# Kernel tuning notes

Hardware: AMD Instinct MI355X
Metric: run time of the kernel (lower is better)

## Reference

```python
import jax, jax.numpy as jnp
import numpy as np
from jax import lax

VOCAB, E, H = 32000, 256, 512
B, T = 64, 1024


def setup_inputs() -> dict:
    key = jax.random.key(0)
    ks = jax.random.split(key, 5)
    tokens = jax.random.randint(ks[0], (B, T), 0, VOCAB, dtype=jnp.int64 if jax.config.jax_enable_x64 else jnp.int32).astype(jnp.int32)
    emb_table = jax.random.normal(ks[1], (VOCAB, E), dtype=jnp.float32) * 0.02
    W_x = jax.random.normal(ks[2], (E, 4 * H), dtype=jnp.float32) * 0.02
    W_h = jax.random.normal(ks[3], (H, 4 * H), dtype=jnp.float32) * 0.02
    b = jnp.zeros((4 * H,), dtype=jnp.float32)
    h0 = jnp.zeros((B, H), dtype=jnp.float32)
    c0 = jnp.zeros((B, H), dtype=jnp.float32)
    return {"tokens": tokens, "h0": h0, "c0": c0, "emb_table": emb_table,
            "W_x": W_x, "W_h": W_h, "b": b}


def reference(tokens, h0, c0, emb_table, W_x, W_h, b):
    # Embedding lookup with mask_zero=True semantics: token 0 is padding.
    x = emb_table[tokens]                      # [B, T, E]
    mask = tokens != 0                         # [B, T]
    # Precompute input projections for all timesteps (same math, one GEMM).
    xz = jnp.einsum('bte,ef->btf', x, W_x) + b  # [B, T, 4H]

    def step(carry, inp):
        h, c = carry
        xzt, mt = inp                          # [B,4H], [B]
        z = xzt + h @ W_h                      # [B, 4H]
        i, f, g, o = jnp.split(z, 4, axis=-1)  # Keras gate order: i, f, c, o
        i = jax.nn.sigmoid(i)
        f = jax.nn.sigmoid(f)
        g = jnp.tanh(g)
        o = jax.nn.sigmoid(o)
        c_new = f * c + i * g
        h_new = o * jnp.tanh(c_new)
        m = mt[:, None]
        # Masked steps carry previous state/output (Keras masking behavior).
        h = jnp.where(m, h_new, h)
        c = jnp.where(m, c_new, c)
        return (h, c), h

    (h_T, c_T), outs = lax.scan(step, (h0, c0),
                                (xz.transpose(1, 0, 2), mask.T))
    return outs.transpose(1, 0, 2), h_T, c_T  # [B,T,H], [B,H], [B,H]
```

## Files before the change

### kernel.cpp

```cpp
#include <hip/hip_runtime.h>
#include <hip/hip_bf16.h>

#define B_ 64
#define T_ 1024
#define E_ 256
#define H_ 512
#define ZN_ 2048
#define NSLICE 64
#define KTX 8
#define KTH 16
#define KT_ (KTX + KTH)

typedef short bf16x8 __attribute__((ext_vector_type(8)));
typedef float f32x4 __attribute__((ext_vector_type(4)));
typedef int i32x4 __attribute__((ext_vector_type(4)));

union frag_u { i32x4 i; bf16x8 h; };

#define RAW_BAR() __builtin_amdgcn_s_barrier()
#define LGKM0() asm volatile("s_waitcnt lgkmcnt(0)" ::: "memory")
#define VM0() asm volatile("s_waitcnt vmcnt(0)" ::: "memory")
#define SCHED_BAR() __builtin_amdgcn_sched_barrier(0)

__device__ __forceinline__ short f2bf(float f) {
  union { float f; unsigned u; } v; v.f = f;
  unsigned r = v.u + 0x7fffu + ((v.u >> 16) & 1u);
  return (short)(r >> 16);
}
__device__ __forceinline__ float sigmoidf_(float x) { return 1.f / (1.f + __expf(-x)); }
__device__ __forceinline__ float tanhf_(float x) {
  x = fminf(10.f, fmaxf(-10.f, x));
  float e = __expf(2.f * x);
  return (e - 1.f) / (e + 1.f);
}

__device__ __forceinline__ i32x4 ld_sys(const void* p) {
  i32x4 r;
  asm volatile("global_load_dwordx4 %0, %1, off sc0 sc1" : "=v"(r) : "v"(p) : "memory");
  return r;
}
__device__ __forceinline__ i32x4 ld_sys16_poll(const void* p) {
  i32x4 r;
  asm volatile("global_load_dwordx4 %0, %1, off sc0 sc1\n\ts_waitcnt vmcnt(0)"
               : "=v"(r) : "v"(p) : "memory");
  return r;
}
__device__ __forceinline__ void st_sys(void* p, i32x4 v) {
  asm volatile("global_store_dwordx4 %0, %1, off sc0 sc1" :: "v"(p), "v"(v) : "memory");
}
__device__ __forceinline__ void st_sys_i32(int* p, int v) {
  asm volatile("global_store_dword %0, %1, off sc0 sc1" :: "v"(p), "v"(v) : "memory");
}


__global__ void k_emb_cvt(const float* __restrict__ emb, short* __restrict__ dst, int n8) {
  int i = blockIdx.x * blockDim.x + threadIdx.x;
  if (i >= n8) return;
  const float4* s = (const float4*)emb;
  float4 a = s[2 * i], b = s[2 * i + 1];
  bf16x8 o;
  o[0] = f2bf(a.x); o[1] = f2bf(a.y); o[2] = f2bf(a.z); o[3] = f2bf(a.w);
  o[4] = f2bf(b.x); o[5] = f2bf(b.y); o[6] = f2bf(b.z); o[7] = f2bf(b.w);
  ((bf16x8*)dst)[i] = o;
}

__global__ void k_wfrag(const float* __restrict__ Wx, const float* __restrict__ Wh,
                        short* __restrict__ wf) {
  int tid = blockIdx.x * blockDim.x + threadIdx.x;
  if (tid >= NSLICE * 2 * KT_ * 64) return;
  int lane = tid & 63;
  int kt = (tid >> 6) % KT_;
  int nt = (tid >> 6) / KT_ % 2;
  int s = tid / (64 * KT_ * 2);
  int c16 = lane & 15, ksub = lane >> 4;
  int g = c16 & 3, hc = c16 >> 2;
  int zcol = g * H_ + s * 8 + nt * 4 + hc;
  int k0 = kt * 32 + ksub * 8;
  bf16x8 o;
#pragma unroll
  for (int i = 0; i < 8; ++i) {
    int k = k0 + i;
    float v = (k < E_) ? Wx[(size_t)k * ZN_ + zcol] : Wh[(size_t)(k - E_) * ZN_ + zcol];
    o[i] = f2bf(v);
  }
  ((bf16x8*)wf)[tid] = o;
}

__global__ void k_tok(const int* __restrict__ tok, int* __restrict__ tokT,
                      unsigned long long* __restrict__ mask) {
  int t = blockIdx.x * blockDim.x + threadIdx.x;
  if (t >= T_) return;
  unsigned long long m = 0ull;
  for (int b = 0; b < B_; ++b) {
    int tk = tok[b * T_ + t];
    tokT[t * B_ + b] = tk;
    if (tk != 0) m |= (1ull << b);
  }
  mask[t] = m;
}

__global__ void k_init(const float* __restrict__ h0, short* __restrict__ hbuf0,
                       int* __restrict__ flags) {
  int i = blockIdx.x * blockDim.x + threadIdx.x;
  if (i < 1024) flags[i] = 0;
  if (i >= B_ * H_) return;
  hbuf0[i] = f2bf(h0[i]);
}


__global__ __launch_bounds__(384, 1) void k_lstm(
    const int* __restrict__ tokT, const short* __restrict__ emb,
    const short* __restrict__ wf, const float* __restrict__ bias,
    const unsigned long long* __restrict__ maskv,
    short* __restrict__ hb0, short* __restrict__ hb1,
    const float* __restrict__ h0, const float* __restrict__ c0,
    float* __restrict__ out, int* __restrict__ tags)
{
  __shared__ __align__(16) short x_wf[2 * KTX * 64 * 8];
  __shared__ __align__(16) float hlocF[2][B_][8];
  __shared__ __align__(16) short hlocBF[B_][8];
  __shared__ int scnt, ocnt;

  int s = blockIdx.x;
  int w = threadIdx.x >> 6, l = threadIdx.x & 63;
  int c16 = l & 15, ksub = l >> 4;
  int g = c16 & 3, hc = c16 >> 2;
  int base = l & ~3;
  int arow = w * 16 + c16;

  if (threadIdx.x == 0) { scnt = 0; ocnt = 0; }

  for (int idx = threadIdx.x; idx < 2 * KTX * 64; idx += 384) {
    int lane = idx & 63;
    int ktn = idx >> 6;
    int nt = ktn / KTX, kt = ktn % KTX;
    ((bf16x8*)x_wf)[idx] = ((const bf16x8*)wf)[(((size_t)(s * 2 + nt)) * KT_ + kt) * 64 + lane];
  }

  bf16x8 wreg0[KTH], wreg1[KTH];
  float zb0 = 0.f, zb1 = 0.f;
  float cst[2][4], hst[2][4];
  if (w < 4) {
    const bf16x8* b0 = (const bf16x8*)wf + (((size_t)(s * 2 + 0)) * KT_ + KTX) * 64 + l;
    const bf16x8* b1 = (const bf16x8*)wf + (((size_t)(s * 2 + 1)) * KT_ + KTX) * 64 + l;
#pragma unroll
    for (int kt = 0; kt < KTH; ++kt) { wreg0[kt] = b0[kt * 64]; wreg1[kt] = b1[kt * 64]; }
    zb0 = bias[g * H_ + s * 8 + 0 + hc];
    zb1 = bias[g * H_ + s * 8 + 4 + hc];
#pragma unroll
    for (int j = 0; j < 2; ++j) {
      int col = s * 8 + j * 4 + hc;
#pragma unroll
      for (int r = 0; r < 4; ++r) {
        int row = w * 16 + ksub * 4 + r;
        cst[j][r] = c0[row * H_ + col];
        hst[j][r] = h0[row * H_ + col];
      }
    }
  }
  LGKM0();
  RAW_BAR();

  f32x4 accx0 = {0.f, 0.f, 0.f, 0.f}, accx1 = {0.f, 0.f, 0.f, 0.f};
  auto compute_x = [&](int t) {
    int tk = tokT[t * B_ + arow];
    const bf16x8* ax = (const bf16x8*)emb + (size_t)tk * 32 + ksub;
    f32x4 a0 = {0.f, 0.f, 0.f, 0.f}, a1 = {0.f, 0.f, 0.f, 0.f};
#pragma unroll
    for (int kt = 0; kt < KTX; ++kt) {
      bf16x8 a = ax[kt * 4];
      a0 = __builtin_amdgcn_mfma_f32_16x16x32_bf16(a, ((const bf16x8*)x_wf)[(0 * KTX + kt) * 64 + l], a0, 0, 0, 0);
      a1 = __builtin_amdgcn_mfma_f32_16x16x32_bf16(a, ((const bf16x8*)x_wf)[(1 * KTX + kt) * 64 + l], a1, 0, 0, 0);
    }
    accx0 = a0; accx1 = a1;
  };

  if (w < 4) compute_x(0);

  if (w < 4) {
    for (int t = 0; t < T_; ++t) {
      int par = t & 1;
      const short* hr = (t & 1) ? hb1 : hb0;
      short* hw       = (t & 1) ? hb0 : hb1;

      if (t > 0) {
        for (;;) {
          i32x4 tg = ld_sys16_poll(tags + l * 4);
          if (__all(tg[0] >= t && tg[1] >= t && tg[2] >= t && tg[3] >= t)) break;
        }
      }

      const short* hbase = hr + arow * H_ + ksub * 8;
      frag_u hf[KTH];
#pragma unroll
      for (int kt = 0; kt < KTH; ++kt) hf[kt].i = ld_sys(hbase + kt * 32);
      VM0();
      SCHED_BAR();

      f32x4 ac0 = accx0, ac1 = accx1;
#pragma unroll
      for (int kt = 0; kt < KTH; ++kt) {
        ac0 = __builtin_amdgcn_mfma_f32_16x16x32_bf16(hf[kt].h, wreg0[kt], ac0, 0, 0, 0);
        ac1 = __builtin_amdgcn_mfma_f32_16x16x32_bf16(hf[kt].h, wreg1[kt], ac1, 0, 0, 0);
      }

      while (__hip_atomic_load(&ocnt, __ATOMIC_ACQUIRE, __HIP_MEMORY_SCOPE_WORKGROUP) < 2 * (t - 1)) {}

      unsigned long long mk = maskv[t];
#pragma unroll
      for (int j = 0; j < 2; ++j) {
        float zb = (j == 0) ? zb0 : zb1;
        int lc = j * 4 + hc;
        float act[4];
#pragma unroll
        for (int r = 0; r < 4; ++r) {
          float z = ((j == 0) ? ac0[r] : ac1[r]) + zb;
          act[r] = (g == 2) ? tanhf_(z) : sigmoidf_(z);
        }
#pragma unroll
        for (int r = 0; r < 4; ++r) {
          float fs = __shfl(act[r], base + 1);
          float gt = __shfl(act[r], base + 2);
          float os = __shfl(act[r], base + 3);
          if (g == 0) {
            int row = w * 16 + ksub * 4 + r;
            bool mm = (mk >> row) & 1ull;
            float cn = fs * cst[j][r] + act[r] * gt;
            float hn = os * tanhf_(cn);
            if (mm) { cst[j][r] = cn; hst[j][r] = hn; }
            hlocF[par][row][lc] = hst[j][r];
            hlocBF[row][lc] = f2bf(hst[j][r]);
          }
        }
      }
      LGKM0();
      SCHED_BAR();

      if (l == 0)
        __hip_atomic_fetch_add(&scnt, 1, __ATOMIC_RELEASE, __HIP_MEMORY_SCOPE_WORKGROUP);

      if (l < 16) {
        frag_u pv; pv.h = *(const bf16x8*)&hlocBF[w * 16 + l][0];
        st_sys(hw + (w * 16 + l) * H_ + s * 8, pv.i);
      }
      if (t == T_ - 1 && g == 0) {
#pragma unroll
        for (int j = 0; j < 2; ++j) {
          int col = s * 8 + j * 4 + hc;
#pragma unroll
          for (int r = 0; r < 4; ++r) {
            int row = w * 16 + ksub * 4 + r;
            out[(size_t)B_ * T_ * H_ + row * H_ + col] = hst[j][r];
            out[(size_t)B_ * T_ * H_ + B_ * H_ + row * H_ + col] = cst[j][r];
          }
        }
      }
      VM0();
      if (l == 0) st_sys_i32(tags + (s * 4 + w), t + 1);

      if (t + 1 < T_) compute_x(t + 1);
    }
  } else {
    for (int t = 0; t < T_; ++t) {
      int par = t & 1;
      while (__hip_atomic_load(&scnt, __ATOMIC_ACQUIRE, __HIP_MEMORY_SCOPE_WORKGROUP) < 4 * (t + 1)) {}
      int row = (w - 4) * 32 + (l >> 1), half = l & 1;
      f32x4 v = *(const f32x4*)&hlocF[par][row][half * 4];
      LGKM0();
      if (l == 0)
        __hip_atomic_fetch_add(&ocnt, 1, __ATOMIC_RELEASE, __HIP_MEMORY_SCOPE_WORKGROUP);
      __builtin_nontemporal_store(v, (f32x4*)(out + ((size_t)row * T_ + t) * H_ + s * 8 + half * 4));
    }
  }
}


extern "C" void kernel_launch(void* const* d_in, const int* in_sizes, int n_in,
                              void* d_out, int out_size, void* d_ws, size_t ws_size,
                              hipStream_t stream) {
  (void)in_sizes; (void)n_in; (void)out_size; (void)ws_size;
  const int* tokens = (const int*)d_in[0];
  const float* h0 = (const float*)d_in[1];
  const float* c0 = (const float*)d_in[2];
  const float* emb = (const float*)d_in[3];
  const float* Wx = (const float*)d_in[4];
  const float* Wh = (const float*)d_in[5];
  const float* bias = (const float*)d_in[6];
  float* out = (float*)d_out;
  char* ws = (char*)d_ws;

  short* emb_bf = (short*)(ws);
  short* wf     = (short*)(ws + 16384000);
  unsigned long long* mask = (unsigned long long*)(ws + 19529728);
  int* tokT     = (int*)(ws + 19537920);
  short* hb0    = (short*)(ws + 19800064);
  short* hb1    = (short*)(ws + 19865600);
  int* tags     = (int*)(ws + 19931136);

  k_emb_cvt<<<(1024000 + 255) / 256, 256, 0, stream>>>(emb, emb_bf, 1024000);
  k_wfrag<<<(NSLICE * 2 * KT_ * 64 + 255) / 256, 256, 0, stream>>>(Wx, Wh, wf);
  k_tok<<<(T_ + 255) / 256, 256, 0, stream>>>(tokens, tokT, mask);
  k_init<<<(B_ * H_ + 255) / 256, 256, 0, stream>>>(h0, hb0, tags);

  k_lstm<<<NSLICE, 384, 0, stream>>>(tokT, emb_bf, wf, bias, mask,
                                     hb0, hb1, h0, c0, out, tags);
}
```

Baseline: 6.563 ms.

## Embed step epoch tags inside hidden-state packets to remove separate flag polling

Replaces the separate per-wave tag flags and the store-wait-flag sequence with hidden-state packets that carry the step number next to the data. Consumers poll the data itself until every packet shows the current epoch, so the flag write, its memory fence, and one round-trip between blocks drop out of each recurrent step. The recurrent weights move from registers into LDS, which frees registers but adds LDS reads on the critical path. Tokens are stored as 16-bit values. The packets double the bytes stored and loaded per step, and polling re-reads the full h fragment on every retry.

```diff
diff --git a/kernel.cpp b/kernel.cpp
--- a/kernel.cpp
+++ b/kernel.cpp
@@ -39,17 +39,8 @@
   asm volatile("global_load_dwordx4 %0, %1, off sc0 sc1" : "=v"(r) : "v"(p) : "memory");
   return r;
 }
-__device__ __forceinline__ i32x4 ld_sys16_poll(const void* p) {
-  i32x4 r;
-  asm volatile("global_load_dwordx4 %0, %1, off sc0 sc1\n\ts_waitcnt vmcnt(0)"
-               : "=v"(r) : "v"(p) : "memory");
-  return r;
-}
 __device__ __forceinline__ void st_sys(void* p, i32x4 v) {
   asm volatile("global_store_dwordx4 %0, %1, off sc0 sc1" :: "v"(p), "v"(v) : "memory");
-}
-__device__ __forceinline__ void st_sys_i32(int* p, int v) {
-  asm volatile("global_store_dword %0, %1, off sc0 sc1" :: "v"(p), "v"(v) : "memory");
 }
 
 
@@ -86,37 +77,45 @@
   ((bf16x8*)wf)[tid] = o;
 }
 
-__global__ void k_tok(const int* __restrict__ tok, int* __restrict__ tokT,
+__global__ void k_tok(const int* __restrict__ tok, unsigned short* __restrict__ tokT,
                       unsigned long long* __restrict__ mask) {
   int t = blockIdx.x * blockDim.x + threadIdx.x;
   if (t >= T_) return;
   unsigned long long m = 0ull;
   for (int b = 0; b < B_; ++b) {
     int tk = tok[b * T_ + t];
-    tokT[t * B_ + b] = tk;
+    tokT[t * B_ + b] = (unsigned short)tk;
     if (tk != 0) m |= (1ull << b);
   }
   mask[t] = m;
 }
 
-__global__ void k_init(const float* __restrict__ h0, short* __restrict__ hbuf0,
-                       int* __restrict__ flags) {
+__global__ void k_init(const float* __restrict__ h0, int* __restrict__ hx) {
   int i = blockIdx.x * blockDim.x + threadIdx.x;
-  if (i < 1024) flags[i] = 0;
-  if (i >= B_ * H_) return;
-  hbuf0[i] = f2bf(h0[i]);
-}
-
-
-__global__ __launch_bounds__(384, 1) void k_lstm(
-    const int* __restrict__ tokT, const short* __restrict__ emb,
+  if (i >= 2 * B_ * 128) return;
+  int par = i >> 13;
+  int row = (i >> 7) & 63;
+  int cg = i & 127;
+  i32x4 g = {0, 0, 0, 0};
+  if (par == 0) {
+    const float* src = h0 + row * H_ + cg * 4;
+    g[0] = ((int)f2bf(src[0]) & 0xffff) | ((int)f2bf(src[1]) << 16);
+    g[1] = ((int)f2bf(src[2]) & 0xffff) | ((int)f2bf(src[3]) << 16);
+  }
+  ((i32x4*)hx)[i] = g;
+}
+
+
+__global__ __launch_bounds__(384, 2) void k_lstm(
+    const unsigned short* __restrict__ tokT, const short* __restrict__ emb,
     const short* __restrict__ wf, const float* __restrict__ bias,
     const unsigned long long* __restrict__ maskv,
-    short* __restrict__ hb0, short* __restrict__ hb1,
+    int* __restrict__ hx,
     const float* __restrict__ h0, const float* __restrict__ c0,
-    float* __restrict__ out, int* __restrict__ tags)
+    float* __restrict__ out)
 {
   __shared__ __align__(16) short x_wf[2 * KTX * 64 * 8];
+  __shared__ __align__(16) short wh_lds[2 * KTH * 64 * 8];
   __shared__ __align__(16) float hlocF[2][B_][8];
   __shared__ __align__(16) short hlocBF[B_][8];
   __shared__ int scnt, ocnt;
@@ -136,15 +135,16 @@
     int nt = ktn / KTX, kt = ktn % KTX;
     ((bf16x8*)x_wf)[idx] = ((const bf16x8*)wf)[(((size_t)(s * 2 + nt)) * KT_ + kt) * 64 + lane];
   }
-
-  bf16x8 wreg0[KTH], wreg1[KTH];
+  for (int idx = threadIdx.x; idx < 2 * KTH * 64; idx += 384) {
+    int lane = idx & 63;
+    int ktn = idx >> 6;
+    int nt = ktn / KTH, kt = ktn % KTH;
+    ((bf16x8*)wh_lds)[idx] = ((const bf16x8*)wf)[(((size_t)(s * 2 + nt)) * KT_ + KTX + kt) * 64 + lane];
+  }
+
   float zb0 = 0.f, zb1 = 0.f;
   float cst[2][4], hst[2][4];
   if (w < 4) {
-    const bf16x8* b0 = (const bf16x8*)wf + (((size_t)(s * 2 + 0)) * KT_ + KTX) * 64 + l;
-    const bf16x8* b1 = (const bf16x8*)wf + (((size_t)(s * 2 + 1)) * KT_ + KTX) * 64 + l;
-#pragma unroll
-    for (int kt = 0; kt < KTH; ++kt) { wreg0[kt] = b0[kt * 64]; wreg1[kt] = b1[kt * 64]; }
     zb0 = bias[g * H_ + s * 8 + 0 + hc];
     zb1 = bias[g * H_ + s * 8 + 4 + hc];
 #pragma unroll
@@ -178,30 +178,40 @@
   if (w < 4) compute_x(0);
 
   if (w < 4) {
+    const bf16x8* whp = (const bf16x8*)wh_lds;
     for (int t = 0; t < T_; ++t) {
       int par = t & 1;
-      const short* hr = (t & 1) ? hb1 : hb0;
-      short* hw       = (t & 1) ? hb0 : hb1;
-
-      if (t > 0) {
-        for (;;) {
-          i32x4 tg = ld_sys16_poll(tags + l * 4);
-          if (__all(tg[0] >= t && tg[1] >= t && tg[2] >= t && tg[3] >= t)) break;
-        }
-      }
-
-      const short* hbase = hr + arow * H_ + ksub * 8;
+
+      const i32x4* gbase = (const i32x4*)hx + ((size_t)par * B_ + arow) * 128 + ksub * 2;
       frag_u hf[KTH];
-#pragma unroll
-      for (int kt = 0; kt < KTH; ++kt) hf[kt].i = ld_sys(hbase + kt * 32);
-      VM0();
-      SCHED_BAR();
+      for (;;) {
+        i32x4 ga[KTH], gb[KTH];
+#pragma unroll
+        for (int kt = 0; kt < KTH; ++kt) {
+          ga[kt] = ld_sys(gbase + kt * 8);
+          gb[kt] = ld_sys(gbase + kt * 8 + 1);
+        }
+        VM0();
+        SCHED_BAR();
+        bool ok = true;
+#pragma unroll
+        for (int kt = 0; kt < KTH; ++kt)
+          ok = ok && ga[kt][2] >= t && gb[kt][2] >= t;
+        if (__all(ok)) {
+#pragma unroll
+          for (int kt = 0; kt < KTH; ++kt) {
+            i32x4 f = {ga[kt][0], ga[kt][1], gb[kt][0], gb[kt][1]};
+            hf[kt].i = f;
+          }
+          break;
+        }
+      }
 
       f32x4 ac0 = accx0, ac1 = accx1;
 #pragma unroll
       for (int kt = 0; kt < KTH; ++kt) {
-        ac0 = __builtin_amdgcn_mfma_f32_16x16x32_bf16(hf[kt].h, wreg0[kt], ac0, 0, 0, 0);
-        ac1 = __builtin_amdgcn_mfma_f32_16x16x32_bf16(hf[kt].h, wreg1[kt], ac1, 0, 0, 0);
+        ac0 = __builtin_amdgcn_mfma_f32_16x16x32_bf16(hf[kt].h, whp[(0 * KTH + kt) * 64 + l], ac0, 0, 0, 0);
+        ac1 = __builtin_amdgcn_mfma_f32_16x16x32_bf16(hf[kt].h, whp[(1 * KTH + kt) * 64 + l], ac1, 0, 0, 0);
       }
 
       while (__hip_atomic_load(&ocnt, __ATOMIC_ACQUIRE, __HIP_MEMORY_SCOPE_WORKGROUP) < 2 * (t - 1)) {}
@@ -239,11 +249,22 @@
       if (l == 0)
         __hip_atomic_fetch_add(&scnt, 1, __ATOMIC_RELEASE, __HIP_MEMORY_SCOPE_WORKGROUP);
 
-      if (l < 16) {
-        frag_u pv; pv.h = *(const bf16x8*)&hlocBF[w * 16 + l][0];
-        st_sys(hw + (w * 16 + l) * H_ + s * 8, pv.i);
-      }
-      if (t == T_ - 1 && g == 0) {
+      if (t + 1 < T_) {
+        if (l < 16) {
+          int row = w * 16 + l;
+          int ep = t + 1;
+          int d0 = *(const int*)&hlocBF[row][0];
+          int d1 = *(const int*)&hlocBF[row][2];
+          int d2 = *(const int*)&hlocBF[row][4];
+          int d3 = *(const int*)&hlocBF[row][6];
+          i32x4 g0 = {d0, d1, ep, 0};
+          i32x4 g1 = {d2, d3, ep, 0};
+          i32x4* gp = (i32x4*)hx + ((size_t)(1 - par) * B_ + row) * 128 + s * 2;
+          st_sys(gp, g0);
+          st_sys(gp + 1, g1);
+        }
+        compute_x(t + 1);
+      } else if (g == 0) {
 #pragma unroll
         for (int j = 0; j < 2; ++j) {
           int col = s * 8 + j * 4 + hc;
@@ -255,10 +276,6 @@
           }
         }
       }
-      VM0();
-      if (l == 0) st_sys_i32(tags + (s * 4 + w), t + 1);
-
-      if (t + 1 < T_) compute_x(t + 1);
     }
   } else {
     for (int t = 0; t < T_; ++t) {
@@ -292,16 +309,14 @@
   short* emb_bf = (short*)(ws);
   short* wf     = (short*)(ws + 16384000);
   unsigned long long* mask = (unsigned long long*)(ws + 19529728);
-  int* tokT     = (int*)(ws + 19537920);
-  short* hb0    = (short*)(ws + 19800064);
-  short* hb1    = (short*)(ws + 19865600);
-  int* tags     = (int*)(ws + 19931136);
+  unsigned short* tokT = (unsigned short*)(ws + 19537920);
+  int* hx       = (int*)(ws + 19668992);
 
   k_emb_cvt<<<(1024000 + 255) / 256, 256, 0, stream>>>(emb, emb_bf, 1024000);
   k_wfrag<<<(NSLICE * 2 * KT_ * 64 + 255) / 256, 256, 0, stream>>>(Wx, Wh, wf);
   k_tok<<<(T_ + 255) / 256, 256, 0, stream>>>(tokens, tokT, mask);
-  k_init<<<(B_ * H_ + 255) / 256, 256, 0, stream>>>(h0, hb0, tags);
+  k_init<<<(2 * B_ * 128 + 255) / 256, 256, 0, stream>>>(h0, hx);
 
   k_lstm<<<NSLICE, 384, 0, stream>>>(tokT, emb_bf, wf, bias, mask,
-                                     hb0, hb1, h0, c0, out, tags);
-}
+                                     hx, h0, c0, out);
+}
```

Result: slower. 12.07 ms (+83.8%).
